# Kernel optimization log

Hardware: AMD Instinct MI355X
Metric: run time of the kernel (lower is better)

## Reference

```python
import jax, jax.numpy as jnp
import numpy as np

M, IN, H, OUT, B = 64, 64, 256, 1, 4096


def setup_inputs() -> dict:
    key = jax.random.key(0)
    ks = jax.random.split(key, 7)
    s1 = 1.0 / np.sqrt(IN)
    s2 = 1.0 / np.sqrt(H)
    return {
        "xs": jax.random.normal(ks[0], (M, B, IN), dtype=jnp.float32),
        "W1": jax.random.uniform(ks[1], (M, IN, H), minval=-s1, maxval=s1, dtype=jnp.float32),
        "b1": jax.random.uniform(ks[2], (M, H), minval=-s1, maxval=s1, dtype=jnp.float32),
        "W2": jax.random.uniform(ks[3], (M, H, H), minval=-s2, maxval=s2, dtype=jnp.float32),
        "b2": jax.random.uniform(ks[4], (M, H), minval=-s2, maxval=s2, dtype=jnp.float32),
        "W3": jax.random.uniform(ks[5], (M, H, OUT), minval=-s2, maxval=s2, dtype=jnp.float32),
        "b3": jax.random.uniform(ks[6], (M, OUT), minval=-s2, maxval=s2, dtype=jnp.float32),
    }


def reference(xs, W1, b1, W2, b2, W3, b3):
    # Batched over models: [M, B, in] x [M, in, h] -> [M, B, h]
    h1 = jax.nn.relu(jnp.einsum("mbi,mih->mbh", xs, W1) + b1[:, None, :])
    h2 = jax.nn.relu(jnp.einsum("mbh,mhk->mbk", h1, W2) + b2[:, None, :])
    out = jnp.einsum("mbh,mho->mbo", h2, W3) + b3[:, None, :]
    return out  # [M, B, out]
```

## Files before the change

kernel.cpp:

```cpp
#include <hip/hip_runtime.h>

#define NMODELS 64
#define BBATCH  4096
#define IN_DIM  64
#define H_DIM   256

typedef __attribute__((ext_vector_type(8))) short short8;
typedef __attribute__((ext_vector_type(4))) float floatx4;

__device__ __forceinline__ unsigned short f2bf(float f) {
    unsigned int u = __builtin_bit_cast(unsigned int, f);
    u += 0x7FFFu + ((u >> 16) & 1u);
    return (unsigned short)(u >> 16);
}

__global__ __launch_bounds__(256) void transpose_cvt(const float* __restrict__ src,
                                                     unsigned short* __restrict__ dst,
                                                     int K, int N) {
    __shared__ float lds[64 * 65];
    const int kt = K >> 6, nt = N >> 6;
    const int t = blockIdx.x;
    const int m = t / (kt * nt);
    const int rem = t - m * (kt * nt);
    const int kb = rem / nt, nb = rem - kb * nt;
    const int tid = threadIdx.x;
    const int c = tid & 63, rq = tid >> 6;

    const float* s = src + ((size_t)m * K + (size_t)kb * 64) * N + nb * 64;
#pragma unroll
    for (int it = 0; it < 16; ++it) {
        int r = it * 4 + rq;
        lds[c * 65 + r] = s[(size_t)r * N + c];
    }
    __syncthreads();
    unsigned short* d = dst + ((size_t)m * N + (size_t)nb * 64) * K + kb * 64;
#pragma unroll
    for (int it = 0; it < 16; ++it) {
        int n = it * 4 + rq;
        d[(size_t)n * K + c] = f2bf(lds[n * 65 + c]);
    }
}

__global__ __launch_bounds__(256, 2) void mlp_fused(
    const float* __restrict__ xs,
    const unsigned short* __restrict__ w1t,
    const float* __restrict__ b1,
    const unsigned short* __restrict__ w2t,
    const float* __restrict__ b2,
    const float* __restrict__ w3,
    const float* __restrict__ b3,
    float* __restrict__ out)
{
    __shared__ unsigned short h1s[64 * 256];
    __shared__ float red[4][64];

    const int bid = blockIdx.x;
    const int m   = bid >> 6;
    const int tb  = bid & 63;
    const int tid = threadIdx.x;
    const int w   = tid >> 6;
    const int lane = tid & 63;
    const int q   = lane >> 4;
    const int c16 = lane & 15;
    const int sw  = c16 & 7;

    const float* xrow = xs + ((size_t)m * BBATCH + (size_t)tb * 64) * IN_DIM;
    const unsigned short* w1p = w1t + (size_t)m * (H_DIM * IN_DIM)
                                + (w * 64 + c16) * IN_DIM + q * 8;

    short8 ax[4][2];
#pragma unroll
    for (int rb = 0; rb < 4; ++rb)
#pragma unroll
        for (int kb = 0; kb < 2; ++kb) {
            const float* xp = xrow + (rb * 16 + c16) * IN_DIM + kb * 32 + q * 8;
            float4 v0 = *(const float4*)xp;
            float4 v1 = *(const float4*)(xp + 4);
            short8 a;
            a[0] = (short)f2bf(v0.x); a[1] = (short)f2bf(v0.y);
            a[2] = (short)f2bf(v0.z); a[3] = (short)f2bf(v0.w);
            a[4] = (short)f2bf(v1.x); a[5] = (short)f2bf(v1.y);
            a[6] = (short)f2bf(v1.z); a[7] = (short)f2bf(v1.w);
            ax[rb][kb] = a;
        }

    floatx4 acc[4][4];
#pragma unroll
    for (int rb = 0; rb < 4; ++rb)
#pragma unroll
        for (int nb = 0; nb < 4; ++nb)
            acc[rb][nb] = (floatx4){0.f, 0.f, 0.f, 0.f};

#pragma unroll
    for (int kb = 0; kb < 2; ++kb) {
        short8 bw[4];
#pragma unroll
        for (int nb = 0; nb < 4; ++nb)
            bw[nb] = *(const short8*)(w1p + nb * (16 * IN_DIM) + kb * 32);
#pragma unroll
        for (int nb = 0; nb < 4; ++nb)
#pragma unroll
            for (int rb = 0; rb < 4; ++rb)
                acc[rb][nb] = __builtin_amdgcn_mfma_f32_16x16x32_bf16(
                    ax[rb][kb], bw[nb], acc[rb][nb], 0, 0, 0);
    }

    const int ncol = w * 64 + c16;
    {
        float b1v[4];
#pragma unroll
        for (int nb = 0; nb < 4; ++nb) b1v[nb] = b1[m * H_DIM + ncol + nb * 16];
#pragma unroll
        for (int rb = 0; rb < 4; ++rb)
#pragma unroll
            for (int nb = 0; nb < 4; ++nb)
#pragma unroll
                for (int r = 0; r < 4; ++r) {
                    float v = fmaxf(acc[rb][nb][r] + b1v[nb], 0.f);
                    int row = rb * 16 + q * 4 + r;
                    int col = ncol + nb * 16;
                    int phys = row * 256 + ((((col >> 3) ^ (row & 7)) << 3) | (col & 7));
                    h1s[phys] = f2bf(v);
                }
    }
    __syncthreads();

#pragma unroll
    for (int rb = 0; rb < 4; ++rb)
#pragma unroll
        for (int nb = 0; nb < 4; ++nb)
            acc[rb][nb] = (floatx4){0.f, 0.f, 0.f, 0.f};

    const unsigned short* w2p = w2t + (size_t)m * (H_DIM * H_DIM)
                                + (w * 64 + c16) * H_DIM + q * 8;
#pragma unroll
    for (int kb = 0; kb < 8; ++kb) {
        short8 av[4], bv[4];
#pragma unroll
        for (int rb = 0; rb < 4; ++rb)
            av[rb] = *(const short8*)&h1s[(rb * 16 + c16) * 256 + (((kb * 4 + q) ^ sw) << 3)];
#pragma unroll
        for (int nb = 0; nb < 4; ++nb)
            bv[nb] = *(const short8*)(w2p + nb * (16 * H_DIM) + kb * 32);
#pragma unroll
        for (int nb = 0; nb < 4; ++nb)
#pragma unroll
            for (int rb = 0; rb < 4; ++rb)
                acc[rb][nb] = __builtin_amdgcn_mfma_f32_16x16x32_bf16(
                    av[rb], bv[nb], acc[rb][nb], 0, 0, 0);
    }

    float b2v[4], w3v[4];
#pragma unroll
    for (int nb = 0; nb < 4; ++nb) {
        b2v[nb] = b2[m * H_DIM + ncol + nb * 16];
        w3v[nb] = w3[m * H_DIM + ncol + nb * 16];
    }
    float p[4][4];
#pragma unroll
    for (int rb = 0; rb < 4; ++rb)
#pragma unroll
        for (int r = 0; r < 4; ++r) p[rb][r] = 0.f;
#pragma unroll
    for (int rb = 0; rb < 4; ++rb)
#pragma unroll
        for (int nb = 0; nb < 4; ++nb)
#pragma unroll
            for (int r = 0; r < 4; ++r) {
                float v = fmaxf(acc[rb][nb][r] + b2v[nb], 0.f);
                p[rb][r] += v * w3v[nb];
            }
#pragma unroll
    for (int off = 1; off < 16; off <<= 1)
#pragma unroll
        for (int rb = 0; rb < 4; ++rb)
#pragma unroll
            for (int r = 0; r < 4; ++r)
                p[rb][r] += __shfl_xor(p[rb][r], off);

    if (c16 == 0) {
#pragma unroll
        for (int rb = 0; rb < 4; ++rb)
#pragma unroll
            for (int r = 0; r < 4; ++r)
                red[w][rb * 16 + q * 4 + r] = p[rb][r];
    }
    __syncthreads();
    if (tid < 64) {
        float s = red[0][tid] + red[1][tid] + red[2][tid] + red[3][tid] + b3[m];
        out[(size_t)m * BBATCH + tb * 64 + tid] = s;
    }
}

extern "C" void kernel_launch(void* const* d_in, const int* in_sizes, int n_in,
                              void* d_out, int out_size, void* d_ws, size_t ws_size,
                              hipStream_t stream) {
    const float* xs = (const float*)d_in[0];
    const float* W1 = (const float*)d_in[1];
    const float* b1 = (const float*)d_in[2];
    const float* W2 = (const float*)d_in[3];
    const float* b2 = (const float*)d_in[4];
    const float* W3 = (const float*)d_in[5];
    const float* b3 = (const float*)d_in[6];
    float* out = (float*)d_out;

    unsigned short* w1t = (unsigned short*)d_ws;
    unsigned short* w2t = w1t + (size_t)NMODELS * H_DIM * IN_DIM;

    transpose_cvt<<<NMODELS * 1 * 4, 256, 0, stream>>>(W1, w1t, IN_DIM, H_DIM);
    transpose_cvt<<<NMODELS * 4 * 4, 256, 0, stream>>>(W2, w2t, H_DIM, H_DIM);
    mlp_fused<<<NMODELS * (BBATCH / 64), 256, 0, stream>>>(xs, w1t, b1, w2t, b2, W3, b3, out);
}
```

Baseline: 215.2 us.

## Drop weight pre-transpose kernels; persistent blocks keep W2 in registers across tiles

After: 244.9 us. 13.8% more time.

```diff
diff --git a/kernel.cpp b/kernel.cpp
--- a/kernel.cpp
+++ b/kernel.cpp
@@ -1,4 +1,5 @@
 #include <hip/hip_runtime.h>
+#include <hip/hip_bf16.h>
 
 #define NMODELS 64
 #define BBATCH  4096
@@ -7,188 +8,182 @@
 
 typedef __attribute__((ext_vector_type(8))) short short8;
 typedef __attribute__((ext_vector_type(4))) float floatx4;
+typedef __attribute__((ext_vector_type(4))) unsigned int uint4v;
+typedef __attribute__((ext_vector_type(2))) unsigned int uint2v;
 
 __device__ __forceinline__ unsigned short f2bf(float f) {
     unsigned int u = __builtin_bit_cast(unsigned int, f);
-    u += 0x7FFFu + ((u >> 16) & 1u);
-    return (unsigned short)(u >> 16);
-}
-
-__global__ __launch_bounds__(256) void transpose_cvt(const float* __restrict__ src,
-                                                     unsigned short* __restrict__ dst,
-                                                     int K, int N) {
-    __shared__ float lds[64 * 65];
-    const int kt = K >> 6, nt = N >> 6;
-    const int t = blockIdx.x;
-    const int m = t / (kt * nt);
-    const int rem = t - m * (kt * nt);
-    const int kb = rem / nt, nb = rem - kb * nt;
-    const int tid = threadIdx.x;
-    const int c = tid & 63, rq = tid >> 6;
-
-    const float* s = src + ((size_t)m * K + (size_t)kb * 64) * N + nb * 64;
-#pragma unroll
-    for (int it = 0; it < 16; ++it) {
-        int r = it * 4 + rq;
-        lds[c * 65 + r] = s[(size_t)r * N + c];
-    }
-    __syncthreads();
-    unsigned short* d = dst + ((size_t)m * N + (size_t)nb * 64) * K + kb * 64;
-#pragma unroll
-    for (int it = 0; it < 16; ++it) {
-        int n = it * 4 + rq;
-        d[(size_t)n * K + c] = f2bf(lds[n * 65 + c]);
-    }
+    return (unsigned short)((u + 0x8000u) >> 16);
+}
+__device__ __forceinline__ unsigned int pkbf(float a, float b) {
+    __hip_bfloat162 h = __float22bfloat162_rn(make_float2(a, b));
+    unsigned int u;
+    __builtin_memcpy(&u, &h, 4);
+    return u;
 }
 
 __global__ __launch_bounds__(256, 2) void mlp_fused(
     const float* __restrict__ xs,
-    const unsigned short* __restrict__ w1t,
+    const float* __restrict__ W1,
     const float* __restrict__ b1,
-    const unsigned short* __restrict__ w2t,
+    const float* __restrict__ W2,
     const float* __restrict__ b2,
-    const float* __restrict__ w3,
+    const float* __restrict__ W3,
     const float* __restrict__ b3,
     float* __restrict__ out)
 {
     __shared__ unsigned short h1s[64 * 256];
     __shared__ float red[4][64];
 
-    const int bid = blockIdx.x;
-    const int m   = bid >> 6;
-    const int tb  = bid & 63;
+    const int bid   = blockIdx.x;
+    const int m     = (bid & 7) * 8 + ((bid >> 3) & 7);
+    const int chunk = bid >> 6;
     const int tid = threadIdx.x;
-    const int w   = tid >> 6;
-    const int lane = tid & 63;
-    const int q   = lane >> 4;
-    const int c16 = lane & 15;
-    const int sw  = c16 & 7;
-
-    const float* xrow = xs + ((size_t)m * BBATCH + (size_t)tb * 64) * IN_DIM;
-    const unsigned short* w1p = w1t + (size_t)m * (H_DIM * IN_DIM)
-                                + (w * 64 + c16) * IN_DIM + q * 8;
-
-    short8 ax[4][2];
-#pragma unroll
-    for (int rb = 0; rb < 4; ++rb)
+    const int w = tid >> 6, lane = tid & 63;
+    const int q = lane >> 4, c16 = lane & 15;
+    const int sw = c16 & 7;
+    const int colbase = w * 64 + c16 * 4;
+
+    const float* W1m = W1 + (size_t)m * IN_DIM * H_DIM;
+    const float* W2m = W2 + (size_t)m * H_DIM * H_DIM;
+    const float b3v = b3[m];
+
+    short8 w2r[8][4];
+#pragma unroll
+    for (int kb = 0; kb < 8; ++kb)
+#pragma unroll
+        for (int jh = 0; jh < 2; ++jh) {
+            float4 f[4];
+#pragma unroll
+            for (int j2 = 0; j2 < 4; ++j2)
+                f[j2] = *(const float4*)(W2m
+                        + (size_t)(kb * 32 + q * 8 + jh * 4 + j2) * H_DIM + colbase);
+#pragma unroll
+            for (int nb = 0; nb < 4; ++nb)
+#pragma unroll
+                for (int j2 = 0; j2 < 4; ++j2)
+                    w2r[kb][nb][jh * 4 + j2] = (short)f2bf(((const float*)&f[j2])[nb]);
+        }
+
+#pragma unroll 1
+    for (int it = 0; it < 8; ++it) {
+        const int tile = chunk * 8 + it;
+        const float* xrow = xs + ((size_t)m * BBATCH + (size_t)tile * 64) * IN_DIM;
+
+        floatx4 acc[4][4];
+#pragma unroll
+        for (int rb = 0; rb < 4; ++rb)
+#pragma unroll
+            for (int nb = 0; nb < 4; ++nb)
+                acc[rb][nb] = (floatx4){0.f, 0.f, 0.f, 0.f};
+
 #pragma unroll
         for (int kb = 0; kb < 2; ++kb) {
-            const float* xp = xrow + (rb * 16 + c16) * IN_DIM + kb * 32 + q * 8;
-            float4 v0 = *(const float4*)xp;
-            float4 v1 = *(const float4*)(xp + 4);
-            short8 a;
-            a[0] = (short)f2bf(v0.x); a[1] = (short)f2bf(v0.y);
-            a[2] = (short)f2bf(v0.z); a[3] = (short)f2bf(v0.w);
-            a[4] = (short)f2bf(v1.x); a[5] = (short)f2bf(v1.y);
-            a[6] = (short)f2bf(v1.z); a[7] = (short)f2bf(v1.w);
-            ax[rb][kb] = a;
-        }
-
-    floatx4 acc[4][4];
-#pragma unroll
-    for (int rb = 0; rb < 4; ++rb)
-#pragma unroll
-        for (int nb = 0; nb < 4; ++nb)
-            acc[rb][nb] = (floatx4){0.f, 0.f, 0.f, 0.f};
-
-#pragma unroll
-    for (int kb = 0; kb < 2; ++kb) {
-        short8 bw[4];
-#pragma unroll
-        for (int nb = 0; nb < 4; ++nb)
-            bw[nb] = *(const short8*)(w1p + nb * (16 * IN_DIM) + kb * 32);
-#pragma unroll
-        for (int nb = 0; nb < 4; ++nb)
-#pragma unroll
-            for (int rb = 0; rb < 4; ++rb)
-                acc[rb][nb] = __builtin_amdgcn_mfma_f32_16x16x32_bf16(
-                    ax[rb][kb], bw[nb], acc[rb][nb], 0, 0, 0);
-    }
-
-    const int ncol = w * 64 + c16;
-    {
-        float b1v[4];
-#pragma unroll
-        for (int nb = 0; nb < 4; ++nb) b1v[nb] = b1[m * H_DIM + ncol + nb * 16];
-#pragma unroll
-        for (int rb = 0; rb < 4; ++rb)
-#pragma unroll
-            for (int nb = 0; nb < 4; ++nb)
+            short8 bw[4];
+#pragma unroll
+            for (int jh = 0; jh < 2; ++jh) {
+                float4 f[4];
+#pragma unroll
+                for (int j2 = 0; j2 < 4; ++j2)
+                    f[j2] = *(const float4*)(W1m
+                            + (size_t)(kb * 32 + q * 8 + jh * 4 + j2) * H_DIM + colbase);
+#pragma unroll
+                for (int nb = 0; nb < 4; ++nb)
+#pragma unroll
+                    for (int j2 = 0; j2 < 4; ++j2)
+                        bw[nb][jh * 4 + j2] = (short)f2bf(((const float*)&f[j2])[nb]);
+            }
+#pragma unroll
+            for (int rb = 0; rb < 4; ++rb) {
+                const float* xp = xrow + (rb * 16 + c16) * IN_DIM + kb * 32 + q * 8;
+                float4 v0 = *(const float4*)xp;
+                float4 v1 = *(const float4*)(xp + 4);
+                uint4v u;
+                u[0] = pkbf(v0.x, v0.y); u[1] = pkbf(v0.z, v0.w);
+                u[2] = pkbf(v1.x, v1.y); u[3] = pkbf(v1.z, v1.w);
+                short8 ax = __builtin_bit_cast(short8, u);
+#pragma unroll
+                for (int nb = 0; nb < 4; ++nb)
+                    acc[rb][nb] = __builtin_amdgcn_mfma_f32_16x16x32_bf16(
+                        ax, bw[nb], acc[rb][nb], 0, 0, 0);
+            }
+        }
+
+        {
+            floatx4 b1v = *(const floatx4*)(b1 + m * H_DIM + colbase);
+#pragma unroll
+            for (int rb = 0; rb < 4; ++rb)
 #pragma unroll
                 for (int r = 0; r < 4; ++r) {
-                    float v = fmaxf(acc[rb][nb][r] + b1v[nb], 0.f);
+                    float v0 = fmaxf(acc[rb][0][r] + b1v[0], 0.f);
+                    float v1 = fmaxf(acc[rb][1][r] + b1v[1], 0.f);
+                    float v2 = fmaxf(acc[rb][2][r] + b1v[2], 0.f);
+                    float v3 = fmaxf(acc[rb][3][r] + b1v[3], 0.f);
+                    uint2v u; u[0] = pkbf(v0, v1); u[1] = pkbf(v2, v3);
                     int row = rb * 16 + q * 4 + r;
-                    int col = ncol + nb * 16;
-                    int phys = row * 256 + ((((col >> 3) ^ (row & 7)) << 3) | (col & 7));
-                    h1s[phys] = f2bf(v);
+                    int ch = (w * 8 + (c16 >> 1)) ^ (row & 7);
+                    *(uint2v*)((char*)h1s + row * 512 + ch * 16 + (c16 & 1) * 8) = u;
                 }
-    }
-    __syncthreads();
-
-#pragma unroll
-    for (int rb = 0; rb < 4; ++rb)
-#pragma unroll
-        for (int nb = 0; nb < 4; ++nb)
-            acc[rb][nb] = (floatx4){0.f, 0.f, 0.f, 0.f};
-
-    const unsigned short* w2p = w2t + (size_t)m * (H_DIM * H_DIM)
-                                + (w * 64 + c16) * H_DIM + q * 8;
-#pragma unroll
-    for (int kb = 0; kb < 8; ++kb) {
-        short8 av[4], bv[4];
-#pragma unroll
-        for (int rb = 0; rb < 4; ++rb)
-            av[rb] = *(const short8*)&h1s[(rb * 16 + c16) * 256 + (((kb * 4 + q) ^ sw) << 3)];
-#pragma unroll
-        for (int nb = 0; nb < 4; ++nb)
-            bv[nb] = *(const short8*)(w2p + nb * (16 * H_DIM) + kb * 32);
-#pragma unroll
-        for (int nb = 0; nb < 4; ++nb)
-#pragma unroll
-            for (int rb = 0; rb < 4; ++rb)
-                acc[rb][nb] = __builtin_amdgcn_mfma_f32_16x16x32_bf16(
-                    av[rb], bv[nb], acc[rb][nb], 0, 0, 0);
-    }
-
-    float b2v[4], w3v[4];
-#pragma unroll
-    for (int nb = 0; nb < 4; ++nb) {
-        b2v[nb] = b2[m * H_DIM + ncol + nb * 16];
-        w3v[nb] = w3[m * H_DIM + ncol + nb * 16];
-    }
-    float p[4][4];
-#pragma unroll
-    for (int rb = 0; rb < 4; ++rb)
-#pragma unroll
-        for (int r = 0; r < 4; ++r) p[rb][r] = 0.f;
-#pragma unroll
-    for (int rb = 0; rb < 4; ++rb)
-#pragma unroll
-        for (int nb = 0; nb < 4; ++nb)
-#pragma unroll
-            for (int r = 0; r < 4; ++r) {
-                float v = fmaxf(acc[rb][nb][r] + b2v[nb], 0.f);
-                p[rb][r] += v * w3v[nb];
-            }
-#pragma unroll
-    for (int off = 1; off < 16; off <<= 1)
-#pragma unroll
-        for (int rb = 0; rb < 4; ++rb)
-#pragma unroll
-            for (int r = 0; r < 4; ++r)
-                p[rb][r] += __shfl_xor(p[rb][r], off);
-
-    if (c16 == 0) {
-#pragma unroll
-        for (int rb = 0; rb < 4; ++rb)
-#pragma unroll
-            for (int r = 0; r < 4; ++r)
-                red[w][rb * 16 + q * 4 + r] = p[rb][r];
-    }
-    __syncthreads();
-    if (tid < 64) {
-        float s = red[0][tid] + red[1][tid] + red[2][tid] + red[3][tid] + b3[m];
-        out[(size_t)m * BBATCH + tb * 64 + tid] = s;
+        }
+        __syncthreads();
+
+#pragma unroll
+        for (int rb = 0; rb < 4; ++rb)
+#pragma unroll
+            for (int nb = 0; nb < 4; ++nb)
+                acc[rb][nb] = (floatx4){0.f, 0.f, 0.f, 0.f};
+
+#pragma unroll
+        for (int kb = 0; kb < 8; ++kb) {
+            short8 av[4];
+#pragma unroll
+            for (int rb = 0; rb < 4; ++rb)
+                av[rb] = *(const short8*)((char*)h1s + (rb * 16 + c16) * 512
+                                          + (((kb * 4 + q) ^ sw) * 16));
+#pragma unroll
+            for (int nb = 0; nb < 4; ++nb)
+#pragma unroll
+                for (int rb = 0; rb < 4; ++rb)
+                    acc[rb][nb] = __builtin_amdgcn_mfma_f32_16x16x32_bf16(
+                        av[rb], w2r[kb][nb], acc[rb][nb], 0, 0, 0);
+        }
+
+        floatx4 b2v = *(const floatx4*)(b2 + m * H_DIM + colbase);
+        floatx4 w3v = *(const floatx4*)(W3 + m * H_DIM + colbase);
+        float p[4][4];
+#pragma unroll
+        for (int rb = 0; rb < 4; ++rb)
+#pragma unroll
+            for (int r = 0; r < 4; ++r) p[rb][r] = 0.f;
+#pragma unroll
+        for (int rb = 0; rb < 4; ++rb)
+#pragma unroll
+            for (int nb = 0; nb < 4; ++nb)
+#pragma unroll
+                for (int r = 0; r < 4; ++r) {
+                    float v = fmaxf(acc[rb][nb][r] + b2v[nb], 0.f);
+                    p[rb][r] += v * w3v[nb];
+                }
+#pragma unroll
+        for (int off = 1; off < 16; off <<= 1)
+#pragma unroll
+            for (int rb = 0; rb < 4; ++rb)
+#pragma unroll
+                for (int r = 0; r < 4; ++r)
+                    p[rb][r] += __shfl_xor(p[rb][r], off);
+
+        if (c16 == 0) {
+#pragma unroll
+            for (int rb = 0; rb < 4; ++rb)
+#pragma unroll
+                for (int r = 0; r < 4; ++r)
+                    red[w][rb * 16 + q * 4 + r] = p[rb][r];
+        }
+        __syncthreads();
+        if (tid < 64) {
+            float s = red[0][tid] + red[1][tid] + red[2][tid] + red[3][tid] + b3v;
+            out[(size_t)m * BBATCH + tile * 64 + tid] = s;
+        }
     }
 }
 
@@ -204,10 +199,5 @@
     const float* b3 = (const float*)d_in[6];
     float* out = (float*)d_out;
 
-    unsigned short* w1t = (unsigned short*)d_ws;
-    unsigned short* w2t = w1t + (size_t)NMODELS * H_DIM * IN_DIM;
-
-    transpose_cvt<<<NMODELS * 1 * 4, 256, 0, stream>>>(W1, w1t, IN_DIM, H_DIM);
-    transpose_cvt<<<NMODELS * 4 * 4, 256, 0, stream>>>(W2, w2t, H_DIM, H_DIM);
-    mlp_fused<<<NMODELS * (BBATCH / 64), 256, 0, stream>>>(xs, w1t, b1, w2t, b2, W3, b3, out);
-}
+    mlp_fused<<<512, 256, 0, stream>>>(xs, W1, b1, W2, b2, W3, b3, out);
+}
```
